# Kernel optimization log

Measured on AMD Instinct MI355X. Metric: run time of the kernel, lower is better.

Reference implementation:

```python
import jax, jax.numpy as jnp
import numpy as np

N, T, P = 4096, 4096, 12  # series, timesteps, seasonality period


def setup_inputs() -> dict:
    key = jax.random.key(0)
    ks = jax.random.split(key, 8)
    return {
        "alpha": jax.random.uniform(ks[0], (N,), dtype=jnp.float32),
        "beta": jax.random.uniform(ks[1], (N,), dtype=jnp.float32),
        "gamma": jax.random.uniform(ks[2], (N,), dtype=jnp.float32),
        "init_level": jax.random.normal(ks[3], (N,), dtype=jnp.float32),
        "init_trend": jax.random.normal(ks[4], (N,), dtype=jnp.float32) * 0.01,
        "init_seasonal": jax.random.normal(ks[5], (N, P), dtype=jnp.float32),
        "obs_noise": jax.random.normal(ks[6], (N, T), dtype=jnp.float32),
        "err": jax.random.normal(ks[7], (N, T), dtype=jnp.float32),
    }


def reference(alpha, beta, gamma, init_level, init_trend, init_seasonal, obs_noise, err):
    """ETS 'AAA' (additive error/trend/seasonal) recurrence, vectorized over N series.

    Per timestep t (matching the torch loop with model_type='AAA'):
      current = level + trend + seasonal[t % P]
      y[t]    = current + obs_noise[t] * 0.1
      level'  = alpha*(current + err[t]) + (1-alpha)*(level + trend)
      trend'  = beta*(level' - level) + (1-beta)*trend
      seasonal[t % P] = gamma*err[t] + (1-gamma)*seasonal[t % P]
    """
    Tlen = obs_noise.shape[1]
    Pn = init_seasonal.shape[1]

    def step(carry, xs):
        level, trend, seasonal = carry  # (N,), (N,), (N, P)
        t, on, e = xs                   # scalar, (N,), (N,)
        idx = t % Pn
        s_t = seasonal[:, idx]
        current = level + trend + s_t
        y = current + on * 0.1
        new_level = alpha * (current + e) + (1.0 - alpha) * (level + trend)
        new_trend = beta * (new_level - level) + (1.0 - beta) * trend
        new_seasonal = seasonal.at[:, idx].set(gamma * e + (1.0 - gamma) * s_t)
        return (new_level, new_trend, new_seasonal), y

    xs = (jnp.arange(Tlen), obs_noise.T, err.T)  # scan over time
    _, ys = jax.lax.scan(step, (init_level, init_trend, init_seasonal), xs)
    return ys.T  # (N, T)
```

## Files before the change

### kernel.cpp

```cpp
#include <hip/hip_runtime.h>

#define DEV static __device__ __forceinline__

#define SKEW(j) ((j) + ((j) >> 5))

__global__ __launch_bounds__(64) void ets_wave(
    const float* __restrict__ alpha_, const float* __restrict__ beta_,
    const float* __restrict__ gamma_, const float* __restrict__ lvl0,
    const float* __restrict__ tr0, const float* __restrict__ seas0,
    const float* __restrict__ obs, const float* __restrict__ err,
    float* __restrict__ out, int T)
{
  __shared__ float er_s[4224];

  const int n = blockIdx.x;
  const int lane = threadIdx.x;

  const float4* ER4 = reinterpret_cast<const float4*>(err + (size_t)n * T);
  const float4* OB4 = reinterpret_cast<const float4*>(obs + (size_t)n * T);
  const int nf4 = T >> 2;

#pragma unroll 4
  for (int i = lane; i < nf4; i += 64) {
    float4 e = ER4[i];
    int j = i << 2;
    er_s[SKEW(j + 0)] = e.x; er_s[SKEW(j + 1)] = e.y;
    er_s[SKEW(j + 2)] = e.z; er_s[SKEW(j + 3)] = e.w;
  }

  const float a = alpha_[n], b = beta_[n], g = gamma_[n];
  const float ab = a * b, ig = 1.0f - g;

  const int nper = T / 12;
  const int base = nper >> 6, rem = nper & 63;
  const int m  = base + (lane < rem ? 1 : 0);
  const int p0 = lane * base + min(lane, rem);
  const int t0 = p0 * 12;

  __syncthreads();

  float l = 0.f, tr = 0.f, s[12];
#pragma unroll
  for (int j = 0; j < 12; ++j) s[j] = 0.f;
  {
    int t = t0;
    for (int u = 0; u < m; ++u, t += 12) {
#pragma unroll
      for (int j = 0; j < 12; ++j) {
        float e = er_s[SKEW(t + j)];
        float se = s[j] + e;
        float lt = l + tr;
        l  = fmaf(a, se, lt);
        tr = fmaf(ab, se, tr);
        s[j] = fmaf(g, e, ig * s[j]);
      }
    }
  }

  float S0 = 0.f, S1 = 0.f, dk = 1.f;
  for (int k = 0; k < m; ++k) { S0 += dk; S1 += (float)k * dk; dk *= ig; }
  float GL = 12.0f * (float)m;
  float Gd = dk;
  float Gf = ab * S0;
  float Gc[12];
#pragma unroll
  for (int j = 0; j < 12; ++j)
    Gc[j] = fmaf(a, S0, ab * ((GL - 1.0f - (float)j) * S0 - 12.0f * S1));
  float Pl = l, Pt = tr, Ps[12];
#pragma unroll
  for (int j = 0; j < 12; ++j) Ps[j] = s[j];

#pragma unroll
  for (int dlt = 1; dlt < 64; dlt <<= 1) {
    float oL  = __shfl_up(GL, dlt, 64);
    float od  = __shfl_up(Gd, dlt, 64);
    float of  = __shfl_up(Gf, dlt, 64);
    float oPl = __shfl_up(Pl, dlt, 64);
    float oPt = __shfl_up(Pt, dlt, 64);
    float oc[12], oPs[12];
#pragma unroll
    for (int j = 0; j < 12; ++j) {
      oc[j]  = __shfl_up(Gc[j], dlt, 64);
      oPs[j] = __shfl_up(Ps[j], dlt, 64);
    }
    if (lane >= dlt) {
      float sum_oPs = 0.f, dot = 0.f;
#pragma unroll
      for (int j = 0; j < 12; ++j) {
        sum_oPs += oPs[j];
        dot = fmaf(Gc[j], oPs[j], dot);
      }
      float nPl = oPl + GL * oPt + dot + Pl;
      float nPt = oPt + Gf * sum_oPs + Pt;
#pragma unroll
      for (int j = 0; j < 12; ++j) {
        Ps[j] = fmaf(Gd, oPs[j], Ps[j]);
        Gc[j] = oc[j] + GL * of + Gc[j] * od;
      }
      Pl = nPl; Pt = nPt;
      Gf = of + Gf * od;
      Gd = od * Gd;
      GL = oL + GL;
    }
  }

  const float l0 = lvl0[n], tr00 = tr0[n];
  float s0[12];
#pragma unroll
  for (int j = 0; j < 12; ++j) s0[j] = seas0[(size_t)n * 12 + j];
  float ss = 0.f, cdot = 0.f;
#pragma unroll
  for (int j = 0; j < 12; ++j) { ss += s0[j]; cdot = fmaf(Gc[j], s0[j], cdot); }
  float yl = l0 + GL * tr00 + cdot + Pl;
  float yt = tr00 + Gf * ss + Pt;
  float ys[12];
#pragma unroll
  for (int j = 0; j < 12; ++j) ys[j] = fmaf(Gd, s0[j], Ps[j]);

  l  = __shfl_up(yl, 1, 64);
  tr = __shfl_up(yt, 1, 64);
#pragma unroll
  for (int j = 0; j < 12; ++j) s[j] = __shfl_up(ys[j], 1, 64);
  if (lane == 0) {
    l = l0; tr = tr00;
#pragma unroll
    for (int j = 0; j < 12; ++j) s[j] = s0[j];
  }

  {
    int t = t0;
    for (int u = 0; u < m; ++u, t += 12) {
#pragma unroll
      for (int j = 0; j < 12; ++j) {
        int ad = SKEW(t + j);
        float e = er_s[ad];
        float lt = l + tr;
        float cur = lt + s[j];
        er_s[ad] = cur;
        float se = s[j] + e;
        l  = fmaf(a, se, lt);
        tr = fmaf(ab, se, tr);
        s[j] = fmaf(g, e, ig * s[j]);
      }
    }
  }
  if (lane == 63) {
    int tt = nper * 12;
    int tail = T - tt;
#pragma unroll
    for (int j = 0; j < 11; ++j) {
      if (j < tail) {
        int ad = SKEW(tt + j);
        float e = er_s[ad];
        float lt = l + tr;
        float cur = lt + s[j];
        er_s[ad] = cur;
        float se = s[j] + e;
        l  = fmaf(a, se, lt);
        tr = fmaf(ab, se, tr);
        s[j] = fmaf(g, e, ig * s[j]);
      }
    }
  }

  __syncthreads();

  float4* Y4 = reinterpret_cast<float4*>(out + (size_t)n * T);
#pragma unroll 4
  for (int i = lane; i < nf4; i += 64) {
    float4 o = OB4[i];
    int j = i << 2;
    float4 v = make_float4(fmaf(o.x, 0.1f, er_s[SKEW(j + 0)]),
                           fmaf(o.y, 0.1f, er_s[SKEW(j + 1)]),
                           fmaf(o.z, 0.1f, er_s[SKEW(j + 2)]),
                           fmaf(o.w, 0.1f, er_s[SKEW(j + 3)]));
    Y4[i] = v;
  }
}

__global__ void ets_gen(
    const float* __restrict__ alpha_, const float* __restrict__ beta_,
    const float* __restrict__ gamma_, const float* __restrict__ lvl0,
    const float* __restrict__ tr0, const float* __restrict__ seas0,
    const float* __restrict__ obs, const float* __restrict__ err,
    float* __restrict__ out, int N, int T, int P)
{
  extern __shared__ float smem[];
  int n = blockIdx.x * blockDim.x + threadIdx.x;
  if (n >= N) return;
  float* s = smem + (size_t)threadIdx.x * P;
  for (int j = 0; j < P; ++j) s[j] = seas0[(size_t)n * P + j];

  float a = alpha_[n], b = beta_[n], g = gamma_[n];
  float ia = 1.0f - a, ib = 1.0f - b, ig = 1.0f - g;
  float level = lvl0[n], trend = tr0[n];

  const float* on = obs + (size_t)n * T;
  const float* er = err + (size_t)n * T;
  float*       yo = out + (size_t)n * T;

  int idx = 0;
  for (int t = 0; t < T; ++t) {
    float onj = on[t], ej = er[t];
    float sj  = s[idx];
    float cur = level + trend + sj;
    yo[t] = fmaf(onj, 0.1f, cur);
    float lt  = level + trend;
    float nl  = fmaf(a, cur + ej, ia * lt);
    float nt  = fmaf(b, nl - level, ib * trend);
    s[idx]    = fmaf(g, ej, ig * sj);
    level = nl; trend = nt;
    if (++idx == P) idx = 0;
  }
}

extern "C" void kernel_launch(void* const* d_in, const int* in_sizes, int n_in,
                              void* d_out, int out_size, void* d_ws, size_t ws_size,
                              hipStream_t stream) {
  (void)n_in; (void)out_size; (void)d_ws; (void)ws_size;
  const float* alpha = (const float*)d_in[0];
  const float* beta  = (const float*)d_in[1];
  const float* gamma = (const float*)d_in[2];
  const float* lvl0  = (const float*)d_in[3];
  const float* tr0   = (const float*)d_in[4];
  const float* seas0 = (const float*)d_in[5];
  const float* obs   = (const float*)d_in[6];
  const float* err   = (const float*)d_in[7];
  float* y = (float*)d_out;

  int N = in_sizes[0];
  int P = in_sizes[5] / N;
  int T = in_sizes[6] / N;

  if (P == 12 && (T % 4) == 0 && T >= 12 && T <= 4096) {
    ets_wave<<<dim3(N), dim3(64), 0, stream>>>(
        alpha, beta, gamma, lvl0, tr0, seas0, obs, err, y, T);
  } else {
    int bs = 64;
    size_t sh = (size_t)bs * (size_t)P * sizeof(float);
    ets_gen<<<dim3((N + bs - 1) / bs), dim3(bs), sh, stream>>>(
        alpha, beta, gamma, lvl0, tr0, seas0, obs, err, y, N, T, P);
  }
}
```

Before: 47.35 us.

## Split each series scan across four wavefronts with cross-wave affine carry combine

```diff
diff --git a/kernel.cpp b/kernel.cpp
--- a/kernel.cpp
+++ b/kernel.cpp
@@ -4,7 +4,7 @@
 
 #define SKEW(j) ((j) + ((j) >> 5))
 
-__global__ __launch_bounds__(64) void ets_wave(
+__global__ __launch_bounds__(256, 6) void ets_wave4(
     const float* __restrict__ alpha_, const float* __restrict__ beta_,
     const float* __restrict__ gamma_, const float* __restrict__ lvl0,
     const float* __restrict__ tr0, const float* __restrict__ seas0,
@@ -12,16 +12,18 @@
     float* __restrict__ out, int T)
 {
   __shared__ float er_s[4224];
+  __shared__ float totals[3][32];
 
   const int n = blockIdx.x;
-  const int lane = threadIdx.x;
+  const int tid = threadIdx.x;
+  const int lane = tid & 63;
+  const int wv = tid >> 6;
 
   const float4* ER4 = reinterpret_cast<const float4*>(err + (size_t)n * T);
   const float4* OB4 = reinterpret_cast<const float4*>(obs + (size_t)n * T);
   const int nf4 = T >> 2;
 
-#pragma unroll 4
-  for (int i = lane; i < nf4; i += 64) {
+  for (int i = tid; i < nf4; i += 256) {
     float4 e = ER4[i];
     int j = i << 2;
     er_s[SKEW(j + 0)] = e.x; er_s[SKEW(j + 1)] = e.y;
@@ -32,9 +34,9 @@
   const float ab = a * b, ig = 1.0f - g;
 
   const int nper = T / 12;
-  const int base = nper >> 6, rem = nper & 63;
-  const int m  = base + (lane < rem ? 1 : 0);
-  const int p0 = lane * base + min(lane, rem);
+  const int base = nper >> 8, rem = nper & 255;
+  const int m  = base + (tid < rem ? 1 : 0);
+  const int p0 = tid * base + min(tid, rem);
   const int t0 = p0 * 12;
 
   __syncthreads();
@@ -104,27 +106,49 @@
     }
   }
 
-  const float l0 = lvl0[n], tr00 = tr0[n];
-  float s0[12];
-#pragma unroll
-  for (int j = 0; j < 12; ++j) s0[j] = seas0[(size_t)n * 12 + j];
+  if (lane == 63 && wv < 3) {
+    float* tw = totals[wv];
+    tw[0] = GL; tw[1] = Gd; tw[2] = Gf; tw[3] = Pl; tw[4] = Pt;
+#pragma unroll
+    for (int j = 0; j < 12; ++j) { tw[5 + j] = Gc[j]; tw[17 + j] = Ps[j]; }
+  }
+  __syncthreads();
+
+  float xl = lvl0[n], xt = tr0[n], xs[12];
+#pragma unroll
+  for (int j = 0; j < 12; ++j) xs[j] = seas0[(size_t)n * 12 + j];
+  for (int v = 0; v < wv; ++v) {
+    const float* tw = totals[v];
+    float ss = 0.f, cdot = 0.f;
+#pragma unroll
+    for (int j = 0; j < 12; ++j) {
+      ss += xs[j];
+      cdot = fmaf(tw[5 + j], xs[j], cdot);
+    }
+    float nxl = xl + tw[0] * xt + cdot + tw[3];
+    float nxt = fmaf(tw[2], ss, xt) + tw[4];
+#pragma unroll
+    for (int j = 0; j < 12; ++j) xs[j] = fmaf(tw[1], xs[j], tw[17 + j]);
+    xl = nxl; xt = nxt;
+  }
+
   float ss = 0.f, cdot = 0.f;
 #pragma unroll
-  for (int j = 0; j < 12; ++j) { ss += s0[j]; cdot = fmaf(Gc[j], s0[j], cdot); }
-  float yl = l0 + GL * tr00 + cdot + Pl;
-  float yt = tr00 + Gf * ss + Pt;
+  for (int j = 0; j < 12; ++j) { ss += xs[j]; cdot = fmaf(Gc[j], xs[j], cdot); }
+  float yl = xl + GL * xt + cdot + Pl;
+  float yt = xt + Gf * ss + Pt;
   float ys[12];
 #pragma unroll
-  for (int j = 0; j < 12; ++j) ys[j] = fmaf(Gd, s0[j], Ps[j]);
+  for (int j = 0; j < 12; ++j) ys[j] = fmaf(Gd, xs[j], Ps[j]);
 
   l  = __shfl_up(yl, 1, 64);
   tr = __shfl_up(yt, 1, 64);
 #pragma unroll
   for (int j = 0; j < 12; ++j) s[j] = __shfl_up(ys[j], 1, 64);
   if (lane == 0) {
-    l = l0; tr = tr00;
-#pragma unroll
-    for (int j = 0; j < 12; ++j) s[j] = s0[j];
+    l = xl; tr = xt;
+#pragma unroll
+    for (int j = 0; j < 12; ++j) s[j] = xs[j];
   }
 
   {
@@ -144,7 +168,7 @@
       }
     }
   }
-  if (lane == 63) {
+  if (tid == 255) {
     int tt = nper * 12;
     int tail = T - tt;
 #pragma unroll
@@ -166,8 +190,7 @@
   __syncthreads();
 
   float4* Y4 = reinterpret_cast<float4*>(out + (size_t)n * T);
-#pragma unroll 4
-  for (int i = lane; i < nf4; i += 64) {
+  for (int i = tid; i < nf4; i += 256) {
     float4 o = OB4[i];
     int j = i << 2;
     float4 v = make_float4(fmaf(o.x, 0.1f, er_s[SKEW(j + 0)]),
@@ -233,7 +256,7 @@
   int T = in_sizes[6] / N;
 
   if (P == 12 && (T % 4) == 0 && T >= 12 && T <= 4096) {
-    ets_wave<<<dim3(N), dim3(64), 0, stream>>>(
+    ets_wave4<<<dim3(N), dim3(256), 0, stream>>>(
         alpha, beta, gamma, lvl0, tr0, seas0, obs, err, y, T);
   } else {
     int bs = 64;
```

Result: slower. 132.5 us (+179.9%).

## Keep per-lane series chunks in registers and compress scan coefficients

Applied to the files above, without the earlier changes.

```diff
diff --git a/kernel.cpp b/kernel.cpp
--- a/kernel.cpp
+++ b/kernel.cpp
@@ -2,31 +2,34 @@
 
 #define DEV static __device__ __forceinline__
 
-#define SKEW(j) ((j) + ((j) >> 5))
-
-__global__ __launch_bounds__(64) void ets_wave(
+DEV float elem(const float4& v, int j) {
+  switch (j & 3) {
+    case 0: return v.x;
+    case 1: return v.y;
+    case 2: return v.z;
+    default: return v.w;
+  }
+}
+DEV void setelem(float4& v, int j, float x) {
+  switch (j & 3) {
+    case 0: v.x = x; break;
+    case 1: v.y = x; break;
+    case 2: v.z = x; break;
+    default: v.w = x; break;
+  }
+}
+
+__global__ __launch_bounds__(64, 3) void ets_reg(
     const float* __restrict__ alpha_, const float* __restrict__ beta_,
     const float* __restrict__ gamma_, const float* __restrict__ lvl0,
     const float* __restrict__ tr0, const float* __restrict__ seas0,
     const float* __restrict__ obs, const float* __restrict__ err,
     float* __restrict__ out, int T)
 {
-  __shared__ float er_s[4224];
+  constexpr int MAXP = 6;
 
   const int n = blockIdx.x;
   const int lane = threadIdx.x;
-
-  const float4* ER4 = reinterpret_cast<const float4*>(err + (size_t)n * T);
-  const float4* OB4 = reinterpret_cast<const float4*>(obs + (size_t)n * T);
-  const int nf4 = T >> 2;
-
-#pragma unroll 4
-  for (int i = lane; i < nf4; i += 64) {
-    float4 e = ER4[i];
-    int j = i << 2;
-    er_s[SKEW(j + 0)] = e.x; er_s[SKEW(j + 1)] = e.y;
-    er_s[SKEW(j + 2)] = e.z; er_s[SKEW(j + 3)] = e.w;
-  }
 
   const float a = alpha_[n], b = beta_[n], g = gamma_[n];
   const float ab = a * b, ig = 1.0f - g;
@@ -35,19 +38,28 @@
   const int base = nper >> 6, rem = nper & 63;
   const int m  = base + (lane < rem ? 1 : 0);
   const int p0 = lane * base + min(lane, rem);
-  const int t0 = p0 * 12;
-
-  __syncthreads();
+  const float* er = err + (size_t)n * T + (size_t)p0 * 12;
+  const float* ob = obs + (size_t)n * T + (size_t)p0 * 12;
+  float*       yo = out + (size_t)n * T + (size_t)p0 * 12;
+
+  float4 E[MAXP * 3];
+#pragma unroll
+  for (int u = 0; u < MAXP; ++u) {
+    if (u < m) {
+      const float4* e4 = reinterpret_cast<const float4*>(er + u * 12);
+      E[u * 3 + 0] = e4[0]; E[u * 3 + 1] = e4[1]; E[u * 3 + 2] = e4[2];
+    }
+  }
 
   float l = 0.f, tr = 0.f, s[12];
 #pragma unroll
   for (int j = 0; j < 12; ++j) s[j] = 0.f;
-  {
-    int t = t0;
-    for (int u = 0; u < m; ++u, t += 12) {
+#pragma unroll
+  for (int u = 0; u < MAXP; ++u) {
+    if (u < m) {
 #pragma unroll
       for (int j = 0; j < 12; ++j) {
-        float e = er_s[SKEW(t + j)];
+        float e  = elem(E[u * 3 + (j >> 2)], j);
         float se = s[j] + e;
         float lt = l + tr;
         l  = fmaf(a, se, lt);
@@ -58,14 +70,14 @@
   }
 
   float S0 = 0.f, S1 = 0.f, dk = 1.f;
-  for (int k = 0; k < m; ++k) { S0 += dk; S1 += (float)k * dk; dk *= ig; }
+#pragma unroll
+  for (int k = 0; k < MAXP; ++k) {
+    if (k < m) { S0 += dk; S1 += (float)k * dk; dk *= ig; }
+  }
   float GL = 12.0f * (float)m;
   float Gd = dk;
   float Gf = ab * S0;
-  float Gc[12];
-#pragma unroll
-  for (int j = 0; j < 12; ++j)
-    Gc[j] = fmaf(a, S0, ab * ((GL - 1.0f - (float)j) * S0 - 12.0f * S1));
+  float GA = fmaf(a, S0, ab * ((GL - 1.0f) * S0 - 12.0f * S1));
   float Pl = l, Pt = tr, Ps[12];
 #pragma unroll
   for (int j = 0; j < 12; ++j) Ps[j] = s[j];
@@ -75,28 +87,25 @@
     float oL  = __shfl_up(GL, dlt, 64);
     float od  = __shfl_up(Gd, dlt, 64);
     float of  = __shfl_up(Gf, dlt, 64);
+    float oA  = __shfl_up(GA, dlt, 64);
     float oPl = __shfl_up(Pl, dlt, 64);
     float oPt = __shfl_up(Pt, dlt, 64);
-    float oc[12], oPs[12];
-#pragma unroll
-    for (int j = 0; j < 12; ++j) {
-      oc[j]  = __shfl_up(Gc[j], dlt, 64);
-      oPs[j] = __shfl_up(Ps[j], dlt, 64);
-    }
+    float oPs[12];
+#pragma unroll
+    for (int j = 0; j < 12; ++j) oPs[j] = __shfl_up(Ps[j], dlt, 64);
     if (lane >= dlt) {
-      float sum_oPs = 0.f, dot = 0.f;
+      float S = 0.f, W = 0.f;
 #pragma unroll
       for (int j = 0; j < 12; ++j) {
-        sum_oPs += oPs[j];
-        dot = fmaf(Gc[j], oPs[j], dot);
-      }
+        S += oPs[j];
+        W = fmaf((float)j, oPs[j], W);
+      }
+      float dot = GA * S - Gf * W;
       float nPl = oPl + GL * oPt + dot + Pl;
-      float nPt = oPt + Gf * sum_oPs + Pt;
-#pragma unroll
-      for (int j = 0; j < 12; ++j) {
-        Ps[j] = fmaf(Gd, oPs[j], Ps[j]);
-        Gc[j] = oc[j] + GL * of + Gc[j] * od;
-      }
+      float nPt = fmaf(Gf, S, oPt) + Pt;
+#pragma unroll
+      for (int j = 0; j < 12; ++j) Ps[j] = fmaf(Gd, oPs[j], Ps[j]);
+      GA = oA + GL * of + GA * od;
       Pl = nPl; Pt = nPt;
       Gf = of + Gf * od;
       Gd = od * Gd;
@@ -108,11 +117,15 @@
   float s0[12];
 #pragma unroll
   for (int j = 0; j < 12; ++j) s0[j] = seas0[(size_t)n * 12 + j];
-  float ss = 0.f, cdot = 0.f;
-#pragma unroll
-  for (int j = 0; j < 12; ++j) { ss += s0[j]; cdot = fmaf(Gc[j], s0[j], cdot); }
+  float ss = 0.f, sw = 0.f;
+#pragma unroll
+  for (int j = 0; j < 12; ++j) {
+    ss += s0[j];
+    sw = fmaf((float)j, s0[j], sw);
+  }
+  float cdot = GA * ss - Gf * sw;
   float yl = l0 + GL * tr00 + cdot + Pl;
-  float yt = tr00 + Gf * ss + Pt;
+  float yt = fmaf(Gf, ss, tr00) + Pt;
   float ys[12];
 #pragma unroll
   for (int j = 0; j < 12; ++j) ys[j] = fmaf(Gd, s0[j], Ps[j]);
@@ -127,54 +140,51 @@
     for (int j = 0; j < 12; ++j) s[j] = s0[j];
   }
 
-  {
-    int t = t0;
-    for (int u = 0; u < m; ++u, t += 12) {
+#pragma unroll
+  for (int u = 0; u < MAXP; ++u) {
+    if (u < m) {
+      const float4* o4 = reinterpret_cast<const float4*>(ob + u * 12);
+      float4 O0 = o4[0], O1 = o4[1], O2 = o4[2];
+      float4 y0, y1, y2;
 #pragma unroll
       for (int j = 0; j < 12; ++j) {
-        int ad = SKEW(t + j);
-        float e = er_s[ad];
-        float lt = l + tr;
+        float e  = elem(E[u * 3 + (j >> 2)], j);
+        float oj = elem(j < 4 ? O0 : (j < 8 ? O1 : O2), j);
+        float lt  = l + tr;
         float cur = lt + s[j];
-        er_s[ad] = cur;
+        float4& yd = (j < 4 ? y0 : (j < 8 ? y1 : y2));
+        setelem(yd, j, fmaf(oj, 0.1f, cur));
         float se = s[j] + e;
         l  = fmaf(a, se, lt);
         tr = fmaf(ab, se, tr);
         s[j] = fmaf(g, e, ig * s[j]);
       }
-    }
-  }
+      float4* y4 = reinterpret_cast<float4*>(yo + u * 12);
+      y4[0] = y0; y4[1] = y1; y4[2] = y2;
+    }
+  }
+
   if (lane == 63) {
     int tt = nper * 12;
     int tail = T - tt;
-#pragma unroll
-    for (int j = 0; j < 11; ++j) {
-      if (j < tail) {
-        int ad = SKEW(tt + j);
-        float e = er_s[ad];
-        float lt = l + tr;
-        float cur = lt + s[j];
-        er_s[ad] = cur;
-        float se = s[j] + e;
-        l  = fmaf(a, se, lt);
-        tr = fmaf(ab, se, tr);
-        s[j] = fmaf(g, e, ig * s[j]);
-      }
-    }
-  }
-
-  __syncthreads();
-
-  float4* Y4 = reinterpret_cast<float4*>(out + (size_t)n * T);
-#pragma unroll 4
-  for (int i = lane; i < nf4; i += 64) {
-    float4 o = OB4[i];
-    int j = i << 2;
-    float4 v = make_float4(fmaf(o.x, 0.1f, er_s[SKEW(j + 0)]),
-                           fmaf(o.y, 0.1f, er_s[SKEW(j + 1)]),
-                           fmaf(o.z, 0.1f, er_s[SKEW(j + 2)]),
-                           fmaf(o.w, 0.1f, er_s[SKEW(j + 3)]));
-    Y4[i] = v;
+    if (tail > 0) {
+      const float* et = err + (size_t)n * T + tt;
+      const float* ot = obs + (size_t)n * T + tt;
+      float*       yt2 = out + (size_t)n * T + tt;
+#pragma unroll
+      for (int j = 0; j < 11; ++j) {
+        if (j < tail) {
+          float e = et[j], oj = ot[j];
+          float lt  = l + tr;
+          float cur = lt + s[j];
+          yt2[j] = fmaf(oj, 0.1f, cur);
+          float se = s[j] + e;
+          l  = fmaf(a, se, lt);
+          tr = fmaf(ab, se, tr);
+          s[j] = fmaf(g, e, ig * s[j]);
+        }
+      }
+    }
   }
 }
 
@@ -233,7 +243,7 @@
   int T = in_sizes[6] / N;
 
   if (P == 12 && (T % 4) == 0 && T >= 12 && T <= 4096) {
-    ets_wave<<<dim3(N), dim3(64), 0, stream>>>(
+    ets_reg<<<dim3(N), dim3(64), 0, stream>>>(
         alpha, beta, gamma, lvl0, tr0, seas0, obs, err, y, T);
   } else {
     int bs = 64;
```

Result: slower. 68.78 us (+45.3%).
